# Performance work log

Measured on AMD Instinct MI355X. Metric: run time of the kernel, lower is better.

## Reference

```python
import jax, jax.numpy as jnp
import numpy as np

B, S = 64, 256
F, H, V = 512, 2048, 32000
PAD = 0
LN_EPS = 1e-5


def setup_inputs() -> dict:
    key = jax.random.key(0)
    ks = jax.random.split(key, 10)
    inputs = jax.random.randint(ks[0], (B, S), 0, V, dtype=jnp.int64)
    targets = jax.random.randint(ks[1], (B, S), 0, V, dtype=jnp.int64)
    # parameters (kaiming-ish / torch-default-ish scales)
    see = jax.random.normal(ks[2], (2 * F, F), jnp.float32) * (2.0 / (2 * F)) ** 0.5
    bias = jnp.zeros((F,), jnp.float32)
    W_in = jax.random.normal(ks[3], (H, F), jnp.float32) * (1.0 / F) ** 0.5
    b_in = jnp.zeros((H,), jnp.float32)
    W_out = jax.random.normal(ks[4], (F, H), jnp.float32) * (1.0 / H) ** 0.5
    b_out = jnp.zeros((F,), jnp.float32)
    ln_g = jnp.ones((F,), jnp.float32)
    ln_b = jnp.zeros((F,), jnp.float32)
    emb = jax.random.normal(ks[5], (V, F), jnp.float32)
    return {"inputs": inputs, "targets": targets, "see": see, "bias": bias,
            "W_in": W_in, "b_in": b_in, "W_out": W_out, "b_out": b_out,
            "ln_g": ln_g, "ln_b": ln_b, "emb": emb}


def _layernorm(x, g, b):
    mu = jnp.mean(x, axis=-1, keepdims=True)
    var = jnp.mean((x - mu) ** 2, axis=-1, keepdims=True)
    return (x - mu) * jax.lax.rsqrt(var + LN_EPS) * g + b


def reference(inputs, targets, see, bias, W_in, b_in, W_out, b_out, ln_g, ln_b, emb):
    emb_m = emb.at[PAD].set(0.0)  # padding_idx row is zero
    inv_sqrt_f = 1.0 / (F ** 0.5)

    def step(state, xy):
        idx, tgt = xy                      # [B], [B]
        vecs = emb_m[idx]                  # [B,F]
        gate = jax.nn.sigmoid(jnp.concatenate([vecs, state], axis=-1) @ see + bias)
        cont = state * gate + vecs * (1.0 - gate)
        h = jax.nn.relu(_layernorm(cont, ln_g, ln_b) @ W_in.T + b_in)
        out = h @ W_out.T + b_out          # [B,F]
        logits = (out @ emb_m.T) * inv_sqrt_f  # [B,V]
        logp = jax.nn.log_softmax(logits, axis=-1)
        nll = -jnp.take_along_axis(logp, tgt[:, None], axis=1)[:, 0]
        mask = (tgt != PAD).astype(logits.dtype)
        li = jnp.sum(nll * mask) / jnp.maximum(jnp.sum(mask), 1.0)
        return cont, li

    xs = (inputs.T, targets.T)  # [S,B]
    _, losses = jax.lax.scan(step, jnp.zeros((inputs.shape[0], F), emb.dtype), xs)
    return jnp.mean(losses)
```

## Files before the change

### kernel.cpp

```cpp
#include <hip/hip_runtime.h>
#include <hip/hip_fp8.h>

#define F_DIM 512
#define H_DIM 2048
#define V_DIM 32000
#define B_DIM 64
#define S_DIM 256
#define ROWS (S_DIM*B_DIM)
#define NT_LOG 250
#define SCALE 0.04419417382415922f
#define LSE_OFF 40.0f

typedef __attribute__((ext_vector_type(8))) short  short8;
typedef __attribute__((ext_vector_type(4))) float  floatx4;
typedef __attribute__((ext_vector_type(4))) int    intx4;
typedef __attribute__((ext_vector_type(8))) int    i32x8;
typedef __attribute__((ext_vector_type(4))) unsigned int uix4;

static __device__ inline unsigned short f2bf(float x){
  unsigned int u = __float_as_uint(x);
  u += 0x7fffu + ((u >> 16) & 1u);
  return (unsigned short)(u >> 16);
}
static __device__ inline float bf2f(unsigned short u){
  return __uint_as_float(((unsigned int)u) << 16);
}
static __device__ inline unsigned char f2fp8(float x){
  __hip_fp8_e4m3 q(x);
  return q.__x;
}
static __device__ inline int sw8(int row, int col){
  int g = (col >> 3) & 7;
  int chunk = ((g >> 1) ^ ((row >> 1) & 3));
  int lob = (g & 1) ^ ((row >> 3) & 1);
  return (col & ~63) | (chunk << 4) | (lob << 3) | (col & 7);
}
static __device__ inline int zvperm(int c){
  return (c & ~63) | ((c & 15) << 2) | ((c >> 4) & 3);
}
static __device__ inline float wsum(float v){
  #pragma unroll
  for(int m = 32; m > 0; m >>= 1) v += __shfl_xor(v, m);
  return v;
}
static __device__ inline void load_lds16(const void* g, void* l){
  __builtin_amdgcn_global_load_lds((const __attribute__((address_space(1))) void*)g,
                                   (__attribute__((address_space(3))) void*)l, 16, 0, 0);
}

__global__ __launch_bounds__(256) void cast_w(const float* __restrict__ src,
                                              unsigned short* __restrict__ dst, int n){
  int i = blockIdx.x*256 + threadIdx.x;
  int stride = gridDim.x*256;
  for(; i < n; i += stride) dst[i] = f2bf(src[i]);
}
__global__ __launch_bounds__(256) void cast_emb(const float* __restrict__ src,
    unsigned short* __restrict__ dst, unsigned char* __restrict__ d8){
  int i = blockIdx.x*256 + threadIdx.x;
  int stride = gridDim.x*256;
  for(; i < V_DIM*F_DIM; i += stride){
    float v = (i < F_DIM) ? 0.f : src[i];
    dst[i] = f2bf(v);
    int row = i >> 9, col = i & 511;
    d8[(long)row*512 + sw8(row, col)] = f2fp8(v);
  }
}

__global__ __launch_bounds__(256) void prep_see(const float* __restrict__ see,
    unsigned short* __restrict__ TT, unsigned char* __restrict__ B8){
  int n = blockIdx.x;
  for(int k = threadIdx.x; k < 512; k += 256){
    TT[n*512 + k] = f2bf(see[(long)k*512 + n]);
    B8[n*512 + k] = f2fp8(see[(long)(512+k)*512 + n]);
  }
}

__global__ __launch_bounds__(256) void gather_vecs(const float* __restrict__ emb,
    const int* __restrict__ inp, unsigned short* __restrict__ V){
  long row = (long)blockIdx.x*4 + (threadIdx.x >> 6);
  int l = threadIdx.x & 63;
  int t = (int)(row >> 6), b = (int)(row & 63);
  int idx = inp[b*S_DIM + t];
  short8 o;
  if (idx == 0){
    #pragma unroll
    for(int i=0;i<8;i++) o[i] = 0;
  } else {
    const float* e = emb + (long)idx*F_DIM + l*8;
    float4 a = *(const float4*)e;
    float4 bq = *(const float4*)(e + 4);
    o[0]=(short)f2bf(a.x); o[1]=(short)f2bf(a.y); o[2]=(short)f2bf(a.z); o[3]=(short)f2bf(a.w);
    o[4]=(short)f2bf(bq.x);o[5]=(short)f2bf(bq.y);o[6]=(short)f2bf(bq.z);o[7]=(short)f2bf(bq.w);
  }
  *(short8*)(V + row*F_DIM + l*8) = o;
}

__global__ __launch_bounds__(512, 1) void recurrence_batch(
    const unsigned int* __restrict__ ZV,
    const unsigned char* __restrict__ W8,
    unsigned short* __restrict__ CONTB)
{
  __shared__ unsigned char stt[2][16][560];

  const int tid = threadIdx.x;
  const int w  = tid >> 6;
  const int l  = tid & 63;
  const int rl = l & 15, rq = l >> 4;
  const int wg = blockIdx.x;
  const int colb = w*64;

  i32x8 Bfr[4][4];
  #pragma unroll
  for(int kt=0;kt<4;kt++)
    #pragma unroll
    for(int tl=0;tl<4;tl++)
      Bfr[kt][tl] = *(const i32x8*)(W8 + (long)(colb + tl*16 + rl)*512 + kt*128 + rq*32);

  float s_old[16];
  #pragma unroll
  for(int i=0;i<16;i++) s_old[i] = 0.f;

  const unsigned int* zbase = ZV + (long)(wg*16 + rq*4)*512 + colb + rl*4;
  unsigned short* cbase = CONTB + ((long)wg*16 + rq*4)*512 + colb + rl;

  uix4 zv[4];
  #pragma unroll
  for(int r=0;r<4;r++) zv[r] = *(const uix4*)(zbase + (long)r*512);

  for(int t = 0; t < S_DIM; t++){
    asm volatile("s_waitcnt lgkmcnt(0)" ::: "memory");
    __builtin_amdgcn_s_barrier();
    asm volatile("" ::: "memory");

    floatx4 acc[4];
    #pragma unroll
    for(int tl=0;tl<4;tl++) acc[tl] = (floatx4)0.f;

    i32x8 afr[4];
    if (t > 0){
      const unsigned char* sb = &stt[(t-1)&1][0][0] + rl*560 + rq*32;
      #pragma unroll
      for(int kt=0;kt<4;kt++){
        intx4 a0 = *(const intx4*)(sb + kt*128);
        intx4 a1 = *(const intx4*)(sb + kt*128 + 16);
        afr[kt] = __builtin_shufflevector(a0, a1, 0,1,2,3,4,5,6,7);
      }
    }

    unsigned short* cw = cbase + (long)t*64*512;
    unsigned char* swb = &stt[t&1][0][0] + rq*4*560 + colb + rl;

    #pragma unroll
    for(int tl=0;tl<4;tl++){
      if (t > 0){
        #pragma unroll
        for(int kt=0;kt<4;kt++)
          acc[tl] = __builtin_amdgcn_mfma_scale_f32_16x16x128_f8f6f4(
                        afr[kt], Bfr[kt][tl], acc[tl],
                        0, 0,
                        0, 0x7f7f7f7f,
                        0, 0x7f7f7f7f);
      }
      float sv[4];
      #pragma unroll
      for(int r=0;r<4;r++){
        unsigned int p = zv[r][tl];
        float z = __uint_as_float(p << 16) + acc[tl][r];
        float v = __uint_as_float(p & 0xffff0000u);
        float e = __expf(-z);
        float g = __builtin_amdgcn_rcpf(1.f + e);
        float s = fmaf(s_old[tl*4+r] - v, g, v);
        s_old[tl*4+r] = s;
        sv[r] = s;
      }
      #pragma unroll
      for(int pr=0; pr<2; pr++){
        unsigned int bfp, f8p;
        asm("v_cvt_pk_bf16_f32 %0, %1, %2" : "=v"(bfp) : "v"(sv[pr*2]), "v"(sv[pr*2+1]));
        asm("v_cvt_pk_fp8_f32 %0, %1, %2"  : "=v"(f8p) : "v"(sv[pr*2]), "v"(sv[pr*2+1]));
        cw[(long)(pr*2)*512   + tl*16] = (unsigned short)(bfp & 0xffffu);
        cw[(long)(pr*2+1)*512 + tl*16] = (unsigned short)(bfp >> 16);
        swb[(pr*2)*560   + tl*16] = (unsigned char)(f8p & 0xffu);
        swb[(pr*2+1)*560 + tl*16] = (unsigned char)((f8p >> 8) & 0xffu);
      }
    }

    if (t+1 < S_DIM){
      const unsigned int* zp = zbase + (long)(t+1)*64*512;
      #pragma unroll
      for(int r=0;r<4;r++) zv[r] = *(const uix4*)(zp + (long)r*512);
    }
  }
}

__global__ __launch_bounds__(256) void ln_kernel(const unsigned short* __restrict__ contb,
    const float* __restrict__ lg, const float* __restrict__ lb,
    unsigned short* __restrict__ xln)
{
  const int wid = threadIdx.x >> 6, l = threadIdx.x & 63;
  const long row = (long)blockIdx.x*4 + wid;
  short8 xv = *(const short8*)(contb + row*F_DIM + l*8);
  float v[8];
  #pragma unroll
  for(int i=0;i<8;i++) v[i] = bf2f((unsigned short)xv[i]);
  float s = 0.f;
  #pragma unroll
  for(int i=0;i<8;i++) s += v[i];
  s = wsum(s);
  float mu = s * (1.f/512.f);
  float q = 0.f;
  #pragma unroll
  for(int i=0;i<8;i++){ float d = v[i]-mu; q += d*d; }
  q = wsum(q);
  float rs = rsqrtf(q*(1.f/512.f) + 1e-5f);
  short8 o;
  #pragma unroll
  for(int i=0;i<8;i++)
    o[i] = (short)f2bf((v[i]-mu)*rs*lg[l*8+i] + lb[l*8+i]);
  *(short8*)(xln + row*F_DIM + l*8) = o;
}

template<int MODE>
__global__ __launch_bounds__(256) void gemm_bt(
    const unsigned short* __restrict__ A,
    const unsigned short* __restrict__ Bm,
    const float* __restrict__ bias,
    unsigned short* __restrict__ C,
    unsigned char* __restrict__ C8,
    const unsigned short* __restrict__ Vsrc,
    unsigned int* __restrict__ ZVout,
    int M, int N, int K, int tiles_m, int tiles_n)
{
  __shared__ short As[128*64];
  __shared__ short Bs[128*64];

  const int bid = blockIdx.x;
  const int mt = bid % tiles_m;
  const int nt = bid / tiles_m;
  const long m0 = (long)mt * 128;
  const long n0 = (long)nt * 128;
  const int tid = threadIdx.x;
  const int l = tid & 63;
  const int wid = tid >> 6;
  const int wr = wid >> 1, wc = wid & 1;
  const int rl = l & 15, rq = l >> 4;

  const short* Ag = (const short*)A + m0 * K;
  const short* Bg = (const short*)Bm + n0 * K;
  const int grow = tid >> 3;
  const int kp = tid & 7;
  const int ksw = (kp ^ (grow & 7)) * 8;

  floatx4 acc[4][4];
  #pragma unroll
  for(int i=0;i<4;i++)
    #pragma unroll
    for(int j=0;j<4;j++) acc[i][j] = (floatx4)0.f;

  for(int k0 = 0; k0 < K; k0 += 64){
    __syncthreads();
    #pragma unroll
    for(int ro = 0; ro < 128; ro += 32){
      load_lds16(Ag + (long)(ro + grow)*K + k0 + ksw, (void*)(As + (ro+grow)*64 + kp*8));
      load_lds16(Bg + (long)(ro + grow)*K + k0 + ksw, (void*)(Bs + (ro+grow)*64 + kp*8));
    }
    __syncthreads();
    #pragma unroll
    for(int kb = 0; kb < 64; kb += 32){
      const int cb = kb >> 3;
      const int cl = ((cb + rq) ^ (rl & 7)) * 8;
      short8 af[4], bfr[4];
      #pragma unroll
      for(int i=0;i<4;i++) af[i]  = *(const short8*)(As + (wr*64 + i*16 + rl)*64 + cl);
      #pragma unroll
      for(int j=0;j<4;j++) bfr[j] = *(const short8*)(Bs + (wc*64 + j*16 + rl)*64 + cl);
      #pragma unroll
      for(int i=0;i<4;i++)
        #pragma unroll
        for(int j=0;j<4;j++)
          acc[i][j] = __builtin_amdgcn_mfma_f32_16x16x32_bf16(af[i], bfr[j], acc[i][j], 0, 0, 0);
    }
  }

  const long mb = m0 + wr*64;
  const long nb = n0 + wc*64;
  #pragma unroll
  for(int j=0;j<4;j++){
    float bj = bias[nb + j*16 + rl];
    #pragma unroll
    for(int i=0;i<4;i++){
      #pragma unroll
      for(int r=0;r<4;r++){
        float v = acc[i][j][r] + bj;
        if (MODE == 0) v = fmaxf(v, 0.f);
        int rowI = (int)(mb + i*16 + rq*4 + r);
        int colI = (int)(nb + j*16 + rl);
        long idx = (long)rowI*N + colI;
        if (MODE == 5){
          ZVout[(long)rowI*N + zvperm(colI)] =
              ((unsigned)Vsrc[idx] << 16) | (unsigned)f2bf(v);
        } else {
          C[idx] = f2bf(v);
          if (MODE == 4) C8[(long)rowI*512 + sw8(rowI, colI)] = f2fp8(v);
        }
      }
    }
  }
}

__global__ __launch_bounds__(256) void gemm_f8_logits(
    const unsigned char* __restrict__ A8,
    const unsigned char* __restrict__ B8,
    float* __restrict__ part,
    int M, int N, int K, int tiles_m, int tiles_n)
{
  __shared__ unsigned char As8[2][128*64];
  __shared__ unsigned char Bs8[2][128*64];
  float (*sm2)[64][2] = (float(*)[64][2])&As8[0][0];

  const int bid = blockIdx.x;
  const int mt = bid % tiles_m;
  const int nt = bid / tiles_m;
  const long m0 = (long)mt * 128;
  const long n0 = (long)nt * 128;
  const int tid = threadIdx.x;
  const int l = tid & 63;
  const int wid = tid >> 6;
  const int wr = wid >> 1, wc = wid & 1;
  const int rl = l & 15, rq = l >> 4;

  const unsigned char* Ag = A8 + m0 * K;
  const unsigned char* Bg = B8 + n0 * K;
  const int grow = tid >> 2;
  const int kp = tid & 3;

  floatx4 acc[4][4];
  #pragma unroll
  for(int i=0;i<4;i++)
    #pragma unroll
    for(int j=0;j<4;j++) acc[i][j] = (floatx4)0.f;

  const int rsw = (rl >> 1) & 3;
  const int rhi = (rl >> 3) & 1;
  unsigned adrA[2][4], adrB[2][4];
  {
    unsigned baseA = (unsigned)(size_t)(__attribute__((address_space(3))) char*)&As8[0][0];
    unsigned baseB = (unsigned)(size_t)(__attribute__((address_space(3))) char*)&Bs8[0][0];
    #pragma unroll
    for(int kb=0; kb<2; kb++){
      int g = (kb << 2) + rq;
      int cl = ((((g >> 1) ^ rsw)) << 4) | (((g & 1) ^ rhi) << 3);
      #pragma unroll
      for(int i=0;i<4;i++) adrA[kb][i] = baseA + (unsigned)((wr*64 + i*16 + rl)*64 + cl);
      #pragma unroll
      for(int j=0;j<4;j++) adrB[kb][j] = baseB + (unsigned)((wc*64 + j*16 + rl)*64 + cl);
    }
  }
  #define DSRD0(dst, adr) asm volatile("ds_read_b64 %0, %1"             : "=v"(dst) : "v"(adr))
  #define DSRD1(dst, adr) asm volatile("ds_read_b64 %0, %1 offset:8192" : "=v"(dst) : "v"(adr))

  const int nkt = K >> 6;

  #define STAGE_F8(bb, kk) do {                                               \
    const long kof = (long)(kk)*64 + kp*16;                                   \
    load_lds16(Ag + (long)grow*K       + kof, (void*)(&As8[bb][grow*64       + kp*16])); \
    load_lds16(Ag + (long)(64+grow)*K  + kof, (void*)(&As8[bb][(64+grow)*64  + kp*16])); \
    load_lds16(Bg + (long)grow*K       + kof, (void*)(&Bs8[bb][grow*64       + kp*16])); \
    load_lds16(Bg + (long)(64+grow)*K  + kof, (void*)(&Bs8[bb][(64+grow)*64  + kp*16])); \
  } while(0)

  #define MFMA16(afq, bfq)                                                    \
    _Pragma("unroll")                                                         \
    for(int i=0;i<4;i++)                                                      \
      _Pragma("unroll")                                                       \
      for(int j=0;j<4;j++)                                                    \
        acc[i][j] = __builtin_amdgcn_mfma_f32_16x16x32_fp8_fp8(afq[i], bfq[j], acc[i][j], 0, 0, 0)

  STAGE_F8(0, 0);
  STAGE_F8(1, 1);

  for(int tp = 0; tp < nkt/2; tp++){
    asm volatile("s_waitcnt vmcnt(4)" ::: "memory");
    __builtin_amdgcn_s_barrier();
    __builtin_amdgcn_sched_barrier(0);

    long af[2][4], bfr[2][4];
    #pragma unroll
    for(int i=0;i<4;i++) DSRD0(af[0][i],  adrA[0][i]);
    #pragma unroll
    for(int i=0;i<4;i++) DSRD0(af[1][i],  adrA[1][i]);
    #pragma unroll
    for(int j=0;j<4;j++) DSRD0(bfr[0][j], adrB[0][j]);
    #pragma unroll
    for(int j=0;j<4;j++) DSRD0(bfr[1][j], adrB[1][j]);

    asm volatile("s_waitcnt lgkmcnt(0)" ::: "memory");
    __builtin_amdgcn_sched_barrier(0);
    __builtin_amdgcn_s_barrier();
    __builtin_amdgcn_sched_barrier(0);

    if (tp < nkt/2 - 1) STAGE_F8(0, 2*tp + 2);

    __builtin_amdgcn_s_setprio(1);
    MFMA16(af[0], bfr[0]);
    MFMA16(af[1], bfr[1]);
    __builtin_amdgcn_s_setprio(0);

    if (tp < nkt/2 - 1) asm volatile("s_waitcnt vmcnt(4)" ::: "memory");
    else                asm volatile("s_waitcnt vmcnt(0)" ::: "memory");
    __builtin_amdgcn_s_barrier();
    __builtin_amdgcn_sched_barrier(0);

    long ag[2][4], bgr[2][4];
    #pragma unroll
    for(int i=0;i<4;i++) DSRD1(ag[0][i],  adrA[0][i]);
    #pragma unroll
    for(int i=0;i<4;i++) DSRD1(ag[1][i],  adrA[1][i]);
    #pragma unroll
    for(int j=0;j<4;j++) DSRD1(bgr[0][j], adrB[0][j]);
    #pragma unroll
    for(int j=0;j<4;j++) DSRD1(bgr[1][j], adrB[1][j]);

    asm volatile("s_waitcnt lgkmcnt(0)" ::: "memory");
    __builtin_amdgcn_sched_barrier(0);
    __builtin_amdgcn_s_barrier();
    __builtin_amdgcn_sched_barrier(0);

    if (tp < nkt/2 - 1) STAGE_F8(1, 2*tp + 3);

    __builtin_amdgcn_s_setprio(1);
    MFMA16(ag[0], bgr[0]);
    MFMA16(ag[1], bgr[1]);
    __builtin_amdgcn_s_setprio(0);
  }
  #undef STAGE_F8
  #undef MFMA16
  #undef DSRD0
  #undef DSRD1

  #pragma unroll
  for(int i=0;i<4;i++){
    #pragma unroll
    for(int r=0;r<4;r++){
      float sv = 0.f;
      #pragma unroll
      for(int j=0;j<4;j++) sv += __expf(acc[i][j][r]*SCALE - LSE_OFF);
      #pragma unroll
      for(int d=1; d<16; d<<=1) sv += __shfl_xor(sv, d);
      if (rl == 0) sm2[wr][i*16 + rq*4 + r][wc] = sv;
    }
  }
  __syncthreads();
  if (tid < 128){
    int wr2 = tid >> 6, rowl = tid & 63;
    part[(m0 + wr2*64 + rowl)*tiles_n + nt] = sm2[wr2][rowl][0] + sm2[wr2][rowl][1];
  }
}

__global__ __launch_bounds__(256) void tlogit_kernel(const unsigned short* __restrict__ outb,
    const unsigned short* __restrict__ embb, const int* __restrict__ tgt,
    float* __restrict__ TL)
{
  long gw = (long)blockIdx.x*4 + (threadIdx.x >> 6);
  int l = threadIdx.x & 63;
  int t = (int)(gw >> 6), b = (int)(gw & 63);
  int tg = tgt[b*S_DIM + t];
  const unsigned short* o = outb + gw*F_DIM;
  const unsigned short* e = embb + (long)tg*F_DIM;
  short8 ov = *(const short8*)(o + l*8);
  short8 ev = *(const short8*)(e + l*8);
  float s = 0.f;
  #pragma unroll
  for(int i=0;i<8;i++) s += bf2f((unsigned short)ov[i]) * bf2f((unsigned short)ev[i]);
  s = wsum(s);
  if (l == 0) TL[gw] = s * SCALE;
}

__global__ __launch_bounds__(256) void lse_kernel(const float* __restrict__ part,
    const float* __restrict__ TL, float* __restrict__ nll)
{
  long row = (long)blockIdx.x*4 + (threadIdx.x >> 6);
  int l = threadIdx.x & 63;
  float S = 0.f;
  for(int c = l; c < NT_LOG; c += 64)
    S += part[row*NT_LOG + c];
  S = wsum(S);
  if (l == 0) nll[row] = (LSE_OFF + logf(S)) - TL[row];
}

__global__ __launch_bounds__(256) void loss_kernel(const float* __restrict__ nll,
    const int* __restrict__ tgt, float* __restrict__ out)
{
  int t = threadIdx.x;
  float s = 0.f; int cnt = 0;
  for(int b = 0; b < B_DIM; b++){
    int v = tgt[b*S_DIM + t];
    if (v != 0){ s += nll[(long)t*B_DIM + b]; cnt++; }
  }
  float li = s / fmaxf((float)cnt, 1.f);
  li = wsum(li);
  __shared__ float red[4];
  if ((t & 63) == 0) red[t >> 6] = li;
  __syncthreads();
  if (t == 0) out[0] = (red[0]+red[1]+red[2]+red[3]) * (1.f/256.f);
}

extern "C" void kernel_launch(void* const* d_in, const int* in_sizes, int n_in,
                              void* d_out, int out_size, void* d_ws, size_t ws_size,
                              hipStream_t stream)
{
  const int*   inp   = (const int*)d_in[0];
  const int*   tgt   = (const int*)d_in[1];
  const float* see   = (const float*)d_in[2];
  const float* bias  = (const float*)d_in[3];
  const float* W_in  = (const float*)d_in[4];
  const float* b_in  = (const float*)d_in[5];
  const float* W_out = (const float*)d_in[6];
  const float* b_out = (const float*)d_in[7];
  const float* ln_g  = (const float*)d_in[8];
  const float* ln_b  = (const float*)d_in[9];
  const float* emb   = (const float*)d_in[10];

  char* p = (char*)d_ws;
  unsigned short* CONTB= (unsigned short*)p; p += (size_t)ROWS*F_DIM*2;
  unsigned short* Hb   = (unsigned short*)p; p += (size_t)ROWS*H_DIM*2;
  unsigned short* OUTb = (unsigned short*)p; p += (size_t)ROWS*F_DIM*2;
  unsigned short* EMBb = (unsigned short*)p; p += (size_t)V_DIM*F_DIM*2;
  unsigned char* EMB8  = (unsigned char*)p;  p += (size_t)V_DIM*F_DIM;
  unsigned short* WINb = (unsigned short*)p; p += (size_t)H_DIM*F_DIM*2;
  unsigned short* WOUTb= (unsigned short*)p; p += (size_t)F_DIM*H_DIM*2;
  float* TL            = (float*)p;          p += (size_t)ROWS*4;
  float* NLL           = (float*)p;          p += (size_t)ROWS*4;
  unsigned short* VECSb= (unsigned short*)p; p += (size_t)ROWS*F_DIM*2;
  unsigned int* ZV     = (unsigned int*)p;   p += (size_t)ROWS*F_DIM*4;
  unsigned short* SEETT= (unsigned short*)p; p += (size_t)F_DIM*F_DIM*2;
  unsigned char* SEEB8 = (unsigned char*)p;  p += (size_t)F_DIM*F_DIM;
  unsigned short* XLN  = (unsigned short*)ZV;
  unsigned char* OUT8  = (unsigned char*)VECSb;
  float* PART          = (float*)Hb;

  cast_emb<<<4096, 256, 0, stream>>>(emb, EMBb, EMB8);
  cast_w<<<2048, 256, 0, stream>>>(W_in,  WINb,  H_DIM*F_DIM);
  cast_w<<<2048, 256, 0, stream>>>(W_out, WOUTb, F_DIM*H_DIM);
  prep_see<<<512, 256, 0, stream>>>(see, SEETT, SEEB8);
  gather_vecs<<<ROWS/4, 256, 0, stream>>>(emb, inp, VECSb);

  gemm_bt<5><<<128*4, 256, 0, stream>>>(VECSb, SEETT, bias, nullptr, nullptr,
                                        VECSb, ZV, ROWS, F_DIM, F_DIM, 128, 4);

  recurrence_batch<<<4, 512, 0, stream>>>(ZV, SEEB8, CONTB);

  ln_kernel<<<ROWS/4, 256, 0, stream>>>(CONTB, ln_g, ln_b, XLN);
  gemm_bt<0><<<128*16, 256, 0, stream>>>(XLN,  WINb,  b_in,  Hb,   nullptr,
                                         nullptr, nullptr, ROWS, H_DIM, F_DIM, 128, 16);
  gemm_bt<4><<<128*4,  256, 0, stream>>>(Hb,   WOUTb, b_out, OUTb, OUT8,
                                         nullptr, nullptr, ROWS, F_DIM, H_DIM, 128, 4);
  tlogit_kernel<<<ROWS/4, 256, 0, stream>>>(OUTb, EMBb, tgt, TL);
  gemm_f8_logits<<<128*NT_LOG, 256, 0, stream>>>(OUT8, EMB8, PART, ROWS, V_DIM, F_DIM, 128, NT_LOG);
  lse_kernel<<<ROWS/4, 256, 0, stream>>>(PART, TL, NLL);
  loss_kernel<<<1, 256, 0, stream>>>(NLL, tgt, (float*)d_out);
}
```

Measured before the change: 1.126 ms.

## Triple-buffer LDS in fp8 logits GEMM to drop one barrier per k-step

Moves the fp8 logits GEMM from a two-stage LDS buffer to a three-stage ring. The prefetch for k-step t+2 is issued right after the barrier, before the LDS reads of step t. This lets each k-step use a single barrier instead of two. The loop is fully unrolled for 8 k-steps, which hardcodes K=512 and raises LDS use per block, possibly lowering occupancy.

Result: slower. 1.165 ms (+3.4%).

```diff
diff --git a/kernel.cpp b/kernel.cpp
--- a/kernel.cpp
+++ b/kernel.cpp
@@ -314,8 +314,8 @@
     float* __restrict__ part,
     int M, int N, int K, int tiles_m, int tiles_n)
 {
-  __shared__ unsigned char As8[2][128*64];
-  __shared__ unsigned char Bs8[2][128*64];
+  __shared__ unsigned char As8[3][128*64];
+  __shared__ unsigned char Bs8[3][128*64];
   float (*sm2)[64][2] = (float(*)[64][2])&As8[0][0];
 
   const int bid = blockIdx.x;
@@ -356,10 +356,17 @@
       for(int j=0;j<4;j++) adrB[kb][j] = baseB + (unsigned)((wc*64 + j*16 + rl)*64 + cl);
     }
   }
-  #define DSRD0(dst, adr) asm volatile("ds_read_b64 %0, %1"             : "=v"(dst) : "v"(adr))
-  #define DSRD1(dst, adr) asm volatile("ds_read_b64 %0, %1 offset:8192" : "=v"(dst) : "v"(adr))
-
-  const int nkt = K >> 6;
+  #define DSRD(dst, adr, OFS) asm volatile("ds_read_b64 %0, %1 offset:" #OFS : "=v"(dst) : "v"(adr))
+  #define READS(OFS) do{                                                      \
+    DSRD(af[0][0], adrA[0][0], OFS); DSRD(af[0][1], adrA[0][1], OFS);         \
+    DSRD(af[0][2], adrA[0][2], OFS); DSRD(af[0][3], adrA[0][3], OFS);         \
+    DSRD(af[1][0], adrA[1][0], OFS); DSRD(af[1][1], adrA[1][1], OFS);         \
+    DSRD(af[1][2], adrA[1][2], OFS); DSRD(af[1][3], adrA[1][3], OFS);         \
+    DSRD(bfr[0][0], adrB[0][0], OFS); DSRD(bfr[0][1], adrB[0][1], OFS);       \
+    DSRD(bfr[0][2], adrB[0][2], OFS); DSRD(bfr[0][3], adrB[0][3], OFS);       \
+    DSRD(bfr[1][0], adrB[1][0], OFS); DSRD(bfr[1][1], adrB[1][1], OFS);       \
+    DSRD(bfr[1][2], adrB[1][2], OFS); DSRD(bfr[1][3], adrB[1][3], OFS);       \
+  } while(0)
 
   #define STAGE_F8(bb, kk) do {                                               \
     const long kof = (long)(kk)*64 + kp*16;                                   \
@@ -379,64 +386,38 @@
   STAGE_F8(0, 0);
   STAGE_F8(1, 1);
 
-  for(int tp = 0; tp < nkt/2; tp++){
-    asm volatile("s_waitcnt vmcnt(4)" ::: "memory");
+  #pragma unroll
+  for(int t = 0; t < 8; t++){
+    if (t < 7) asm volatile("s_waitcnt vmcnt(4)" ::: "memory");
+    else       asm volatile("s_waitcnt vmcnt(0)" ::: "memory");
     __builtin_amdgcn_s_barrier();
     __builtin_amdgcn_sched_barrier(0);
 
+    if (t + 2 < 8){
+      const int sb = (t + 2) % 3;
+      if (sb == 0)      STAGE_F8(0, t+2);
+      else if (sb == 1) STAGE_F8(1, t+2);
+      else              STAGE_F8(2, t+2);
+    }
+
     long af[2][4], bfr[2][4];
-    #pragma unroll
-    for(int i=0;i<4;i++) DSRD0(af[0][i],  adrA[0][i]);
-    #pragma unroll
-    for(int i=0;i<4;i++) DSRD0(af[1][i],  adrA[1][i]);
-    #pragma unroll
-    for(int j=0;j<4;j++) DSRD0(bfr[0][j], adrB[0][j]);
-    #pragma unroll
-    for(int j=0;j<4;j++) DSRD0(bfr[1][j], adrB[1][j]);
+    const int bi = t % 3;
+    if (bi == 0)      READS(0);
+    else if (bi == 1) READS(8192);
+    else              READS(16384);
 
     asm volatile("s_waitcnt lgkmcnt(0)" ::: "memory");
     __builtin_amdgcn_sched_barrier(0);
-    __builtin_amdgcn_s_barrier();
-    __builtin_amdgcn_sched_barrier(0);
-
-    if (tp < nkt/2 - 1) STAGE_F8(0, 2*tp + 2);
 
     __builtin_amdgcn_s_setprio(1);
     MFMA16(af[0], bfr[0]);
     MFMA16(af[1], bfr[1]);
     __builtin_amdgcn_s_setprio(0);
-
-    if (tp < nkt/2 - 1) asm volatile("s_waitcnt vmcnt(4)" ::: "memory");
-    else                asm volatile("s_waitcnt vmcnt(0)" ::: "memory");
-    __builtin_amdgcn_s_barrier();
-    __builtin_amdgcn_sched_barrier(0);
-
-    long ag[2][4], bgr[2][4];
-    #pragma unroll
-    for(int i=0;i<4;i++) DSRD1(ag[0][i],  adrA[0][i]);
-    #pragma unroll
-    for(int i=0;i<4;i++) DSRD1(ag[1][i],  adrA[1][i]);
-    #pragma unroll
-    for(int j=0;j<4;j++) DSRD1(bgr[0][j], adrB[0][j]);
-    #pragma unroll
-    for(int j=0;j<4;j++) DSRD1(bgr[1][j], adrB[1][j]);
-
-    asm volatile("s_waitcnt lgkmcnt(0)" ::: "memory");
-    __builtin_amdgcn_sched_barrier(0);
-    __builtin_amdgcn_s_barrier();
-    __builtin_amdgcn_sched_barrier(0);
-
-    if (tp < nkt/2 - 1) STAGE_F8(1, 2*tp + 3);
-
-    __builtin_amdgcn_s_setprio(1);
-    MFMA16(ag[0], bgr[0]);
-    MFMA16(ag[1], bgr[1]);
-    __builtin_amdgcn_s_setprio(0);
   }
   #undef STAGE_F8
   #undef MFMA16
-  #undef DSRD0
-  #undef DSRD1
+  #undef READS
+  #undef DSRD
 
   #pragma unroll
   for(int i=0;i<4;i++){
```
